# Kernel optimization log

Hardware: AMD Instinct MI355X
Metric: run time of the kernel (lower is better)

Reference implementation:

```python
import jax, jax.numpy as jnp
import numpy as np

K = 5                # hardcoded top-k in the module's knn branch
KNN_WEIGHT = 1.0     # graph_construct_methods['knn']
NEG_SLOPE = 0.01     # F.leaky_relu default


def setup_inputs() -> dict:
    key = jax.random.key(0)
    # x: [seq_len=12, batch=16, n_nodes=2048, dim=128]
    x = jax.random.normal(key, (12, 16, 2048, 128), dtype=jnp.float32)
    return {"x": x}


def reference(x) -> jnp.ndarray:
    T, B, N, D = x.shape
    # static path: permute to [B, N, T, D] and flatten per-node features -> [B, N, T*D]
    xf = jnp.transpose(x, (1, 2, 0, 3)).reshape(B, N, T * D)
    # cosine similarity: row-normalize then pairwise GEMM -> [B, N, N]
    xn = xf / jnp.linalg.norm(xf, axis=-1, keepdims=True)
    dist = jnp.einsum('bnd,bmd->bnm', xn, xn)
    # top-k along last dim, scatter values into a zero matrix (sparse knn graph)
    knn_val, knn_ind = jax.lax.top_k(dist, K)           # [B, N, K]
    bi = jnp.arange(B)[:, None, None]
    ri = jnp.arange(N)[None, :, None]
    adj = jnp.zeros_like(dist).at[bi, ri, knn_ind].set(knn_val)
    # leaky_relu, method weight
    adj = jnp.where(adj >= 0, adj, NEG_SLOPE * adj) * KNN_WEIGHT
    # symmetric=True
    graphs = (adj + jnp.swapaxes(adj, -2, -1)) * 0.5
    return graphs
```

## Files before the change

kernel.cpp:

```cpp
#include <hip/hip_runtime.h>
#include <math.h>

#define TT 12
#define BB 16
#define NN 2048
#define DD 128
#define FDIM 1536
#define KTOP 5
#define NCAND 8
#define NROWS (BB * NN)
#define NTRI 136
#define OUTSZ (BB * NN * NN)

typedef __attribute__((ext_vector_type(8))) short short8;
typedef __attribute__((ext_vector_type(4))) float f32x4;
typedef const __attribute__((address_space(1))) void* gas_ptr;
typedef __attribute__((address_space(3))) void* las_ptr;

__device__ __forceinline__ unsigned short f2bf(float f) {
    unsigned u = __float_as_uint(f);
    return (unsigned short)((u + 0x7fffu + ((u >> 16) & 1u)) >> 16);
}
__device__ __forceinline__ unsigned short bf2key(unsigned short h) {
    return (unsigned short)(h ^ (0x8000u | (0xFFFFu * (h >> 15))));
}

__device__ __forceinline__ bool tk_better(float v1, int i1, float v2, int i2) {
    return (v1 > v2) || (v1 == v2 && i1 < i2);
}
template <int K>
__device__ __forceinline__ void tk_insert(float bv[K], int bi[K], float v, int idx) {
    if (!tk_better(v, idx, bv[K - 1], bi[K - 1])) return;
    bv[K - 1] = v; bi[K - 1] = idx;
#pragma unroll
    for (int k = K - 1; k > 0; --k) {
        if (tk_better(bv[k], bi[k], bv[k - 1], bi[k - 1])) {
            float tv = bv[k]; bv[k] = bv[k - 1]; bv[k - 1] = tv;
            int tx = bi[k]; bi[k] = bi[k - 1]; bi[k - 1] = tx;
        }
    }
}

__global__ __launch_bounds__(256) void zero_kernel(float4* __restrict__ out) {
    size_t base = (size_t)blockIdx.x * 2048 + threadIdx.x;
    float4 z = make_float4(0.f, 0.f, 0.f, 0.f);
#pragma unroll
    for (int k = 0; k < 8; ++k) out[base + (size_t)k * 256] = z;
}

__global__ __launch_bounds__(256) void normconv_kernel(const float* __restrict__ x,
                                                       float* __restrict__ invn,
                                                       unsigned short* __restrict__ hi) {
    int lane = threadIdx.x & 63;
    int row  = (blockIdx.x << 2) + (threadIdx.x >> 6);
    int b = row >> 11;
    int n = row & (NN - 1);
    float4 f[6];
    float s = 0.0f;
#pragma unroll
    for (int p = 0; p < 6; ++p) {
        int e = ((p << 6) + lane) << 2;
        int t = e >> 7, d = e & 127;
        f[p] = *(const float4*)(x + ((((size_t)t * BB + b) * NN + n) << 7) + d);
        s += f[p].x * f[p].x + f[p].y * f[p].y + f[p].z * f[p].z + f[p].w * f[p].w;
    }
#pragma unroll
    for (int off = 1; off < 64; off <<= 1) s += __shfl_xor(s, off);
    float inv = 1.0f / sqrtf(s);
    if (lane == 0) invn[row] = inv;
    unsigned short* hr = hi + (size_t)row * FDIM;
#pragma unroll
    for (int p = 0; p < 6; ++p) {
        int e = ((p << 6) + lane) << 2;
        ushort4 o;
        o.x = f2bf(f[p].x * inv); o.y = f2bf(f[p].y * inv);
        o.z = f2bf(f[p].z * inv); o.w = f2bf(f[p].w * inv);
        *(ushort4*)(hr + e) = o;
    }
}

__global__ __launch_bounds__(256, 3) void gemm_kernel(const unsigned short* __restrict__ hi,
                                                      unsigned short* __restrict__ dist) {
    __shared__ short As[128 * 64];
    __shared__ short Bs[128 * 64];

    int t = blockIdx.x % NTRI;
    int b = blockIdx.x / NTRI;
    int i = 0;
    while (i < 15 && ((i + 1) * (33 - (i + 1))) / 2 <= t) ++i;
    int j = i + (t - (i * (33 - i)) / 2);
    int n0 = i << 7, m0 = j << 7;

    int tid = threadIdx.x;
    int w = tid >> 6, l = tid & 63;

    int offG[4], offL[4];
#pragma unroll
    for (int g = 0; g < 4; ++g) {
        int s = g * 256 + tid;
        int m = s >> 3;
        int c = (s - m) & 7;
        offG[g] = m * FDIM + (c << 3);
        offL[g] = (g << 12) + (w << 10);
    }
    const unsigned short* gA = hi + ((size_t)(b << 11) + n0) * FDIM;
    const unsigned short* gB = hi + ((size_t)(b << 11) + m0) * FDIM;

    int aSlot[4][2], bSlot[4][2];
#pragma unroll
    for (int a = 0; a < 4; ++a)
#pragma unroll
        for (int ki = 0; ki < 2; ++ki) {
            int c  = (ki << 2) + (l >> 4);
            int ma = ((w >> 1) << 6) + (a << 4) + (l & 15);
            int mb = ((w & 1) << 6) + (a << 4) + (l & 15);
            aSlot[a][ki] = (ma << 3) + ((c + ma) & 7);
            bSlot[a][ki] = (mb << 3) + ((c + mb) & 7);
        }

    f32x4 acc[4][4];
#pragma unroll
    for (int a = 0; a < 4; ++a)
#pragma unroll
        for (int c = 0; c < 4; ++c) acc[a][c] = (f32x4){0.f, 0.f, 0.f, 0.f};

    for (int kc = 0; kc < 24; ++kc) {
        int ko = kc << 6;
        __syncthreads();
#pragma unroll
        for (int g = 0; g < 4; ++g) {
            __builtin_amdgcn_global_load_lds((gas_ptr)(gA + ko + offG[g]),
                                             (las_ptr)((char*)As + offL[g]), 16, 0, 0);
            __builtin_amdgcn_global_load_lds((gas_ptr)(gB + ko + offG[g]),
                                             (las_ptr)((char*)Bs + offL[g]), 16, 0, 0);
        }
        __syncthreads();

        short8 af[4][2], bf[4][2];
#pragma unroll
        for (int a = 0; a < 4; ++a)
#pragma unroll
            for (int ki = 0; ki < 2; ++ki) {
                af[a][ki] = *(const short8*)&As[aSlot[a][ki] << 3];
                bf[a][ki] = *(const short8*)&Bs[bSlot[a][ki] << 3];
            }
#pragma unroll
        for (int ki = 0; ki < 2; ++ki)
#pragma unroll
            for (int a = 0; a < 4; ++a)
#pragma unroll
                for (int c = 0; c < 4; ++c)
                    acc[a][c] = __builtin_amdgcn_mfma_f32_16x16x32_bf16(
                        af[a][ki], bf[c][ki], acc[a][c], 0, 0, 0);
    }

    unsigned short* db = dist + ((size_t)b << 22);
    int rowb = n0 + ((w >> 1) << 6);
    int colb = m0 + ((w & 1) << 6);
#pragma unroll
    for (int a = 0; a < 4; ++a) {
        int r0 = rowb + (a << 4) + ((l >> 4) << 2);
#pragma unroll
        for (int c = 0; c < 4; ++c) {
            int c0 = colb + (c << 4) + (l & 15);
            unsigned short h0 = bf2key(f2bf(acc[a][c][0]));
            unsigned short h1 = bf2key(f2bf(acc[a][c][1]));
            unsigned short h2 = bf2key(f2bf(acc[a][c][2]));
            unsigned short h3 = bf2key(f2bf(acc[a][c][3]));
            db[(size_t)(r0 + 0) * NN + c0] = h0;
            db[(size_t)(r0 + 1) * NN + c0] = h1;
            db[(size_t)(r0 + 2) * NN + c0] = h2;
            db[(size_t)(r0 + 3) * NN + c0] = h3;
            if (i != j) {
                ushort4 o; o.x = h0; o.y = h1; o.z = h2; o.w = h3;
                *(ushort4*)(db + (size_t)c0 * NN + r0) = o;
            }
        }
    }
}

__global__ __launch_bounds__(256) void topk_kernel(const unsigned short* __restrict__ dist,
                                                   int* __restrict__ cand) {
    int wave = threadIdx.x >> 6, lane = threadIdx.x & 63;
    int row  = (blockIdx.x << 2) + wave;
    const unsigned short* p = dist + ((size_t)row << 11);

    unsigned gk[4];
#pragma unroll
    for (int it = 0; it < 4; ++it) {
        int m = (it << 9) + (lane << 3);
        uint4 w2 = *(const uint4*)(p + m);
        unsigned idxv = 2047u - (unsigned)m;
        unsigned best = (w2.x << 16) | idxv;
        unsigned k;
        k = (w2.x & 0xFFFF0000u) | (idxv - 1); best = best > k ? best : k;
        k = (w2.y << 16) | (idxv - 2);         best = best > k ? best : k;
        k = (w2.y & 0xFFFF0000u) | (idxv - 3); best = best > k ? best : k;
        k = (w2.z << 16) | (idxv - 4);         best = best > k ? best : k;
        k = (w2.z & 0xFFFF0000u) | (idxv - 5); best = best > k ? best : k;
        k = (w2.w << 16) | (idxv - 6);         best = best > k ? best : k;
        k = (w2.w & 0xFFFF0000u) | (idxv - 7); best = best > k ? best : k;
        gk[it] = best;
    }

    unsigned mywg = 0;
#pragma unroll
    for (int pass = 0; pass < 8; ++pass) {
        unsigned mx0 = gk[0] > gk[1] ? gk[0] : gk[1];
        unsigned mx1 = gk[2] > gk[3] ? gk[2] : gk[3];
        unsigned mx = mx0 > mx1 ? mx0 : mx1;
#pragma unroll
        for (int off = 1; off < 64; off <<= 1) {
            unsigned o = (unsigned)__shfl_xor((int)mx, off);
            mx = mx > o ? mx : o;
        }
        if (lane == pass) mywg = mx;
#pragma unroll
        for (int tt = 0; tt < 4; ++tt)
            if (gk[tt] == mx) gk[tt] = 0;
    }

    unsigned gkey = (unsigned)__shfl((int)mywg, lane >> 3);
    int gm = 2047 - (int)(gkey & 0x7FFu);
    int m  = ((gm >> 3) << 3) + (lane & 7);
    unsigned key = ((unsigned)p[m] << 16) | (unsigned)(2047 - m);
    int mycand = 0;
#pragma unroll
    for (int pass = 0; pass < 8; ++pass) {
        unsigned mx = key;
#pragma unroll
        for (int off = 1; off < 64; off <<= 1) {
            unsigned o = (unsigned)__shfl_xor((int)mx, off);
            mx = mx > o ? mx : o;
        }
        if (lane == pass) mycand = 2047 - (int)(mx & 0x7FFu);
        if (key == mx) key = 0;
    }
    if (lane < 8) cand[row * NCAND + lane] = mycand;
}

__global__ __launch_bounds__(256, 4) void rescore_kernel(const float* __restrict__ x,
                                                         const float* __restrict__ invn,
                                                         const int* __restrict__ cand,
                                                         float* __restrict__ out) {
    int wave = threadIdx.x >> 6, l = threadIdx.x & 63;
    int row  = (blockIdx.x << 2) + wave;
    int b = row >> 11, n = row & (NN - 1);

    int4 c0 = *(const int4*)(cand + row * NCAND);
    int4 c1 = *(const int4*)(cand + row * NCAND + 4);
    int cix[NCAND] = {c0.x, c0.y, c0.z, c0.w, c1.x, c1.y, c1.z, c1.w};

    float acc[NCAND];
#pragma unroll
    for (int c = 0; c < NCAND; ++c) acc[c] = 0.0f;

#pragma unroll 2
    for (int p = 0; p < 6; ++p) {
        int e = ((p << 6) + l) << 2;
        int t = e >> 7, d = e & 127;
        const float* base = x + ((((size_t)t * BB + b) * NN) << 7) + d;
        float4 fn = *(const float4*)(base + ((size_t)n << 7));
        float4 v[NCAND];
#pragma unroll
        for (int c = 0; c < NCAND; ++c)
            v[c] = *(const float4*)(base + ((size_t)cix[c] << 7));
#pragma unroll
        for (int c = 0; c < NCAND; ++c)
            acc[c] += fn.x * v[c].x + fn.y * v[c].y + fn.z * v[c].z + fn.w * v[c].w;
    }

#pragma unroll
    for (int off = 1; off < 64; off <<= 1) {
#pragma unroll
        for (int c = 0; c < NCAND; ++c) acc[c] += __shfl_xor(acc[c], off);
    }

    if (l == 0) {
        float sn = invn[row];
        float bv[KTOP]; int bi[KTOP];
#pragma unroll
        for (int k = 0; k < KTOP; ++k) { bv[k] = -3.0e38f; bi[k] = 1 << 30; }
#pragma unroll
        for (int c = 0; c < NCAND; ++c) {
            float v = acc[c] * sn * invn[(b << 11) + cix[c]];
            tk_insert<KTOP>(bv, bi, v, cix[c]);
        }
        float* base = out + ((size_t)b << 22);
#pragma unroll
        for (int k = 0; k < KTOP; ++k) {
            float v = bv[k];
            int m = bi[k];
            float a = (v >= 0.0f ? v : 0.01f * v) * 0.5f;
            atomicAdd(base + ((size_t)n << 11) + m, a);
            atomicAdd(base + ((size_t)m << 11) + n, a);
        }
    }
}

extern "C" void kernel_launch(void* const* d_in, const int* in_sizes, int n_in,
                              void* d_out, int out_size, void* d_ws, size_t ws_size,
                              hipStream_t stream) {
    const float* x = (const float*)d_in[0];
    float* out = (float*)d_out;

    unsigned short* dist = (unsigned short*)d_out;
    unsigned short* hi   = (unsigned short*)((char*)d_out + 134217728);

    float* invn = (float*)d_ws;
    int*   cand = (int*)(invn + NROWS);

    normconv_kernel<<<NROWS / 4, 256, 0, stream>>>(x, invn, hi);
    gemm_kernel<<<NTRI * BB, 256, 0, stream>>>(hi, dist);
    topk_kernel<<<NROWS / 4, 256, 0, stream>>>(dist, cand);
    zero_kernel<<<OUTSZ / (256 * 32), 256, 0, stream>>>((float4*)out);
    rescore_kernel<<<NROWS / 4, 256, 0, stream>>>(x, invn, cand, out);
}
```

Baseline: 783.6 us.

## Rewrite Gram GEMM as 256x256 tiles with 8-wave multi-stage LDS pipeline

Replaces the 128x128 triangular-tile GEMM with 256x256 tiles and 512-thread blocks. Global-to-LDS loads now run through a multi-stage ring in 128 KB of LDS, interleaved with MFMA quads. The schedule uses explicit vmcnt/lgkmcnt waits, barriers, setprio, and an XCD-aware block swizzle. The larger tiles are meant to raise reuse and hide load latency. In exchange, the grid drops to 576 blocks, which risks poor wave balance across CUs, and the hand-tuned wait counts add fragility.

Measured after the change: 755.1 us. -3.6%, faster.

```diff
diff --git a/kernel.cpp b/kernel.cpp
--- a/kernel.cpp
+++ b/kernel.cpp
@@ -9,7 +9,7 @@
 #define KTOP 5
 #define NCAND 8
 #define NROWS (BB * NN)
-#define NTRI 136
+#define NTRI256 36
 #define OUTSZ (BB * NN * NN)
 
 typedef __attribute__((ext_vector_type(8))) short short8;
@@ -79,99 +79,147 @@
     }
 }
 
-__global__ __launch_bounds__(256, 3) void gemm_kernel(const unsigned short* __restrict__ hi,
+
+__device__ __forceinline__ void stage2(const unsigned short* __restrict__ hi, char* lds,
+                                       unsigned so, int d) {
+    __builtin_amdgcn_global_load_lds((gas_ptr)(hi + so),           (las_ptr)(lds + d),        16, 0, 0);
+    __builtin_amdgcn_global_load_lds((gas_ptr)(hi + so + 98304u),  (las_ptr)(lds + d + 8192), 16, 0, 0);
+}
+
+__device__ __forceinline__ void load_frags(const char* lds, int aB, int bB, int baseA,
+                                           short8 (&af)[2][8], short8 (&bf)[2][4]) {
+#pragma unroll
+    for (int kk = 0; kk < 2; ++kk) {
+        int ba = baseA ^ (kk << 6);
+#pragma unroll
+        for (int m = 0; m < 8; ++m)
+            af[kk][m] = *(const short8*)(lds + aB + ba + (m << 11));
+#pragma unroll
+        for (int n = 0; n < 4; ++n)
+            bf[kk][n] = *(const short8*)(lds + bB + ba + (n << 11));
+    }
+}
+
+template <int MH, int NH>
+__device__ __forceinline__ void quad(f32x4 (&acc)[8][4], const short8 (&af)[2][8],
+                                     const short8 (&bf)[2][4]) {
+#pragma unroll
+    for (int kk = 0; kk < 2; ++kk)
+#pragma unroll
+        for (int m = 0; m < 4; ++m)
+#pragma unroll
+            for (int n = 0; n < 2; ++n)
+                acc[MH * 4 + m][NH * 2 + n] = __builtin_amdgcn_mfma_f32_16x16x32_bf16(
+                    af[kk][MH * 4 + m], bf[kk][NH * 2 + n], acc[MH * 4 + m][NH * 2 + n], 0, 0, 0);
+}
+
+#define VM6 asm volatile("s_waitcnt vmcnt(6)" ::: "memory")
+#define VM0 asm volatile("s_waitcnt vmcnt(0)" ::: "memory")
+#define LG0 do { asm volatile("s_waitcnt lgkmcnt(0)" ::: "memory"); \
+                 __builtin_amdgcn_sched_barrier(0); } while (0)
+#define BAR __builtin_amdgcn_s_barrier()
+#define PRI1 __builtin_amdgcn_s_setprio(1)
+#define PRI0 __builtin_amdgcn_s_setprio(0)
+
+__global__ __launch_bounds__(512, 2) void gemm_kernel(const unsigned short* __restrict__ hi,
                                                       unsigned short* __restrict__ dist) {
-    __shared__ short As[128 * 64];
-    __shared__ short Bs[128 * 64];
-
-    int t = blockIdx.x % NTRI;
-    int b = blockIdx.x / NTRI;
-    int i = 0;
-    while (i < 15 && ((i + 1) * (33 - (i + 1))) / 2 <= t) ++i;
-    int j = i + (t - (i * (33 - i)) / 2);
-    int n0 = i << 7, m0 = j << 7;
+    __shared__ char lds[131072];
+
+    int bid = blockIdx.x;
+    int swz = (bid & 7) * 72 + (bid >> 3);
+    int b   = swz / NTRI256;
+    int t   = swz - b * NTRI256;
+    int ti = 0;
+    while (ti < 7 && (ti + 1) * (17 - (ti + 1)) / 2 <= t) ++ti;
+    int tj = ti + (t - ti * (17 - ti) / 2);
 
     int tid = threadIdx.x;
-    int w = tid >> 6, l = tid & 63;
-
-    int offG[4], offL[4];
-#pragma unroll
-    for (int g = 0; g < 4; ++g) {
-        int s = g * 256 + tid;
-        int m = s >> 3;
-        int c = (s - m) & 7;
-        offG[g] = m * FDIM + (c << 3);
-        offL[g] = (g << 12) + (w << 10);
-    }
-    const unsigned short* gA = hi + ((size_t)(b << 11) + n0) * FDIM;
-    const unsigned short* gB = hi + ((size_t)(b << 11) + m0) * FDIM;
-
-    int aSlot[4][2], bSlot[4][2];
-#pragma unroll
-    for (int a = 0; a < 4; ++a)
-#pragma unroll
-        for (int ki = 0; ki < 2; ++ki) {
-            int c  = (ki << 2) + (l >> 4);
-            int ma = ((w >> 1) << 6) + (a << 4) + (l & 15);
-            int mb = ((w & 1) << 6) + (a << 4) + (l & 15);
-            aSlot[a][ki] = (ma << 3) + ((c + ma) & 7);
-            bSlot[a][ki] = (mb << 3) + ((c + mb) & 7);
-        }
-
-    f32x4 acc[4][4];
-#pragma unroll
-    for (int a = 0; a < 4; ++a)
-#pragma unroll
-        for (int c = 0; c < 4; ++c) acc[a][c] = (f32x4){0.f, 0.f, 0.f, 0.f};
-
-    for (int kc = 0; kc < 24; ++kc) {
-        int ko = kc << 6;
-        __syncthreads();
-#pragma unroll
-        for (int g = 0; g < 4; ++g) {
-            __builtin_amdgcn_global_load_lds((gas_ptr)(gA + ko + offG[g]),
-                                             (las_ptr)((char*)As + offL[g]), 16, 0, 0);
-            __builtin_amdgcn_global_load_lds((gas_ptr)(gB + ko + offG[g]),
-                                             (las_ptr)((char*)Bs + offL[g]), 16, 0, 0);
-        }
-        __syncthreads();
-
-        short8 af[4][2], bf[4][2];
-#pragma unroll
-        for (int a = 0; a < 4; ++a)
-#pragma unroll
-            for (int ki = 0; ki < 2; ++ki) {
-                af[a][ki] = *(const short8*)&As[aSlot[a][ki] << 3];
-                bf[a][ki] = *(const short8*)&Bs[bSlot[a][ki] << 3];
-            }
-#pragma unroll
-        for (int ki = 0; ki < 2; ++ki)
-#pragma unroll
-            for (int a = 0; a < 4; ++a)
-#pragma unroll
-                for (int c = 0; c < 4; ++c)
-                    acc[a][c] = __builtin_amdgcn_mfma_f32_16x16x32_bf16(
-                        af[a][ki], bf[c][ki], acc[a][c], 0, 0, 0);
-    }
+    int l   = tid & 63;
+    int ws  = __builtin_amdgcn_readfirstlane(tid >> 6);
+    int wr  = ws >> 2, wc = ws & 3;
+    int l15 = l & 15, lhi = l >> 4;
+
+    int lr0 = tid >> 3;
+    int g0  = (tid - lr0) & 7;
+    unsigned offA = (((unsigned)b << 11) + ((unsigned)ti << 8) + lr0) * FDIM + g0 * 8;
+    unsigned offB = (((unsigned)b << 11) + ((unsigned)tj << 8) + lr0) * FDIM + g0 * 8;
+    int dst0 = tid << 4;
+
+    int baseA = l15 * 128 + (((lhi + l15) & 7) << 4);
+    int aB0 = wr << 14,  aB1 = (4 | wr) << 14;
+    int bB0 = ((2 | (wc >> 1)) << 14) + ((wc & 1) << 13);
+    int bB1 = bB0 + (4 << 14);
+
+    f32x4 acc[8][4];
+#pragma unroll
+    for (int m = 0; m < 8; ++m)
+#pragma unroll
+        for (int n = 0; n < 4; ++n) acc[m][n] = (f32x4){0.f, 0.f, 0.f, 0.f};
+    short8 af[2][8], bf[2][4];
+
+    stage2(hi, lds, offA,                 dst0 + (0 << 14));
+    stage2(hi, lds, offA + 196608u,       dst0 + (1 << 14));
+    stage2(hi, lds, offB,                 dst0 + (2 << 14));
+    stage2(hi, lds, offB + 196608u,       dst0 + (3 << 14));
+    stage2(hi, lds, offA + 64u,           dst0 + (4 << 14));
+    stage2(hi, lds, offA + 196608u + 64u, dst0 + (5 << 14));
+    stage2(hi, lds, offB + 64u,           dst0 + (6 << 14));
+    VM6; BAR;
+
+#pragma unroll 1
+    for (int it = 0; it < 11; ++it) {
+        unsigned k1 = (unsigned)(it * 128 + 64);
+        unsigned k2 = k1 + 64, k3 = k1 + 128;
+        load_frags(lds, aB0, bB0, baseA, af, bf);
+        stage2(hi, lds, offB + 196608u + k1, dst0 + (7 << 14));
+        BAR; LG0; PRI1; quad<0, 0>(acc, af, bf); PRI0; BAR;
+        stage2(hi, lds, offA + k2,           dst0 + (0 << 14));
+        BAR; PRI1; quad<0, 1>(acc, af, bf); PRI0; BAR;
+        stage2(hi, lds, offA + 196608u + k2, dst0 + (1 << 14));
+        BAR; PRI1; quad<1, 1>(acc, af, bf); PRI0; BAR;
+        stage2(hi, lds, offB + k2,           dst0 + (2 << 14));
+        VM6;
+        BAR; PRI1; quad<1, 0>(acc, af, bf); PRI0; BAR;
+        load_frags(lds, aB1, bB1, baseA, af, bf);
+        stage2(hi, lds, offB + 196608u + k2, dst0 + (3 << 14));
+        BAR; LG0; PRI1; quad<0, 0>(acc, af, bf); PRI0; BAR;
+        stage2(hi, lds, offA + k3,           dst0 + (4 << 14));
+        BAR; PRI1; quad<0, 1>(acc, af, bf); PRI0; BAR;
+        stage2(hi, lds, offA + 196608u + k3, dst0 + (5 << 14));
+        BAR; PRI1; quad<1, 1>(acc, af, bf); PRI0; BAR;
+        stage2(hi, lds, offB + k3,           dst0 + (6 << 14));
+        VM6;
+        BAR; PRI1; quad<1, 0>(acc, af, bf); PRI0; BAR;
+    }
+    load_frags(lds, aB0, bB0, baseA, af, bf);
+    stage2(hi, lds, offB + 196608u + 1472u, dst0 + (7 << 14));
+    BAR; LG0;
+    PRI1; quad<0, 0>(acc, af, bf); quad<0, 1>(acc, af, bf);
+    quad<1, 1>(acc, af, bf); quad<1, 0>(acc, af, bf); PRI0;
+    VM0; BAR;
+    load_frags(lds, aB1, bB1, baseA, af, bf);
+    LG0;
+    PRI1; quad<0, 0>(acc, af, bf); quad<0, 1>(acc, af, bf);
+    quad<1, 1>(acc, af, bf); quad<1, 0>(acc, af, bf); PRI0;
 
     unsigned short* db = dist + ((size_t)b << 22);
-    int rowb = n0 + ((w >> 1) << 6);
-    int colb = m0 + ((w & 1) << 6);
-#pragma unroll
-    for (int a = 0; a < 4; ++a) {
-        int r0 = rowb + (a << 4) + ((l >> 4) << 2);
-#pragma unroll
-        for (int c = 0; c < 4; ++c) {
-            int c0 = colb + (c << 4) + (l & 15);
-            unsigned short h0 = bf2key(f2bf(acc[a][c][0]));
-            unsigned short h1 = bf2key(f2bf(acc[a][c][1]));
-            unsigned short h2 = bf2key(f2bf(acc[a][c][2]));
-            unsigned short h3 = bf2key(f2bf(acc[a][c][3]));
+    int rowb = (ti << 8) + (wr << 7);
+    int colb = (tj << 8) + (wc << 6);
+#pragma unroll
+    for (int m = 0; m < 8; ++m) {
+        int r0 = rowb + (m << 4) + (lhi << 2);
+#pragma unroll
+        for (int n = 0; n < 4; ++n) {
+            int c0 = colb + (n << 4) + l15;
+            unsigned short h0 = bf2key(f2bf(acc[m][n][0]));
+            unsigned short h1 = bf2key(f2bf(acc[m][n][1]));
+            unsigned short h2 = bf2key(f2bf(acc[m][n][2]));
+            unsigned short h3 = bf2key(f2bf(acc[m][n][3]));
             db[(size_t)(r0 + 0) * NN + c0] = h0;
             db[(size_t)(r0 + 1) * NN + c0] = h1;
             db[(size_t)(r0 + 2) * NN + c0] = h2;
             db[(size_t)(r0 + 3) * NN + c0] = h3;
-            if (i != j) {
+            if (ti != tj) {
                 ushort4 o; o.x = h0; o.y = h1; o.z = h2; o.w = h3;
                 *(ushort4*)(db + (size_t)c0 * NN + r0) = o;
             }
@@ -311,7 +359,7 @@
     int*   cand = (int*)(invn + NROWS);
 
     normconv_kernel<<<NROWS / 4, 256, 0, stream>>>(x, invn, hi);
-    gemm_kernel<<<NTRI * BB, 256, 0, stream>>>(hi, dist);
+    gemm_kernel<<<NTRI256 * BB, 512, 0, stream>>>(hi, dist);
     topk_kernel<<<NROWS / 4, 256, 0, stream>>>(dist, cand);
     zero_kernel<<<OUTSZ / (256 * 32), 256, 0, stream>>>((float4*)out);
     rescore_kernel<<<NROWS / 4, 256, 0, stream>>>(x, invn, cand, out);
```
